# Kernel tuning notes

Hardware: AMD Instinct MI355X
Metric: run time of the kernel (lower is better)

The kernel has to match this reference:

```python
import jax, jax.numpy as jnp
import numpy as np

B, E, N, M = 512, 1024, 1024, 128
EPS = 1e-16


def setup_inputs() -> dict:
    key = jax.random.key(0)
    k1, k2, k3, k4 = jax.random.split(key, 4)
    embeddings = jax.random.normal(k1, (B, E), dtype=jnp.float32)
    w_prev = jax.random.uniform(k2, (B, N), dtype=jnp.float32)
    w_prev = w_prev / jnp.sum(w_prev, axis=1, keepdims=True)  # valid attention over N slots
    memory = jax.random.normal(k3, (B, N, M), dtype=jnp.float32)
    W = jax.random.normal(k4, (E, M + 6), dtype=jnp.float32) * (1.4 / np.sqrt(0.5 * (E + M + 6)))
    b = jnp.zeros((M + 6,), dtype=jnp.float32)
    return {"embeddings": embeddings, "w_prev": w_prev, "memory": memory, "W": W, "b": b}


def reference(embeddings, w_prev, memory, W, b):
    # Dense projection to (k | beta | g | s | y), widths (M, 1, 1, 3, 1)
    params = embeddings @ W + b  # [B, M+6]
    k = params[:, :M]                       # content key [B, M]
    beta = jax.nn.softplus(params[:, M:M + 1])   # key strength >= 0
    g = jax.nn.sigmoid(params[:, M + 1:M + 2])   # interpolation gate in (0,1)
    s = jax.nn.softmax(params[:, M + 2:M + 5], axis=1)  # shift weights [B, 3]
    y = 1.0 + jax.nn.softplus(params[:, M + 5:M + 6])   # sharpening >= 1

    # Content addressing: cosine similarity of key vs each memory row
    dot = jnp.einsum('bm,bnm->bn', k, memory)  # [B, N]
    k_norm = jnp.linalg.norm(k, axis=1, keepdims=True)          # [B, 1]
    m_norm = jnp.linalg.norm(memory, axis=2)                    # [B, N]
    cos = dot / (k_norm * m_norm + EPS)
    w_c = jax.nn.softmax(beta * cos, axis=1)  # [B, N]

    # Interpolate with previous weighting
    w_g = g * w_c + (1.0 - g) * w_prev

    # Circular convolution with 3-tap shift kernel (shifts -1, 0, +1)
    w_tilde = (s[:, 0:1] * jnp.roll(w_g, 1, axis=1)
               + s[:, 1:2] * w_g
               + s[:, 2:3] * jnp.roll(w_g, -1, axis=1))

    # Sharpen
    w_pow = jnp.power(w_tilde + EPS, y)
    w = w_pow / jnp.sum(w_pow, axis=1, keepdims=True)  # memory_locations [B, N]

    # Memory read: weighted sum of rows
    memory_data = jnp.einsum('bn,bnm->bm', w, memory)  # [B, M]
    return (memory_data, w)
```

## Files before the change

### kernel.cpp

```cpp
#include <hip/hip_runtime.h>
#include <hip/hip_bf16.h>

#define B_ 512
#define E_ 1024
#define N_ 1024
#define M_ 128
#define P_ 134

#define RLO 24
#define LLO 18

__device__ __forceinline__ float softplus_f(float x) {
    return fmaxf(x, 0.f) + log1pf(expf(-fabsf(x)));
}

__global__ __launch_bounds__(256) void k_params(
    const float* __restrict__ emb, const float* __restrict__ W,
    const float* __restrict__ bias,
    float* __restrict__ k_all, float* __restrict__ knorm,
    float* __restrict__ scal)
{
    __shared__ float se[E_];
    __shared__ float sp[P_];
    __shared__ float red[2];
    const int b = blockIdx.x, t = threadIdx.x;
    for (int i = t; i < E_; i += 256) se[i] = emb[b * E_ + i];
    __syncthreads();
    if (t < P_) {
        float a0 = 0.f, a1 = 0.f, a2 = 0.f, a3 = 0.f;
        #pragma unroll 4
        for (int e = 0; e < E_; e += 4) {
            a0 = fmaf(se[e + 0], W[(e + 0) * P_ + t], a0);
            a1 = fmaf(se[e + 1], W[(e + 1) * P_ + t], a1);
            a2 = fmaf(se[e + 2], W[(e + 2) * P_ + t], a2);
            a3 = fmaf(se[e + 3], W[(e + 3) * P_ + t], a3);
        }
        sp[t] = bias[t] + ((a0 + a1) + (a2 + a3));
    }
    __syncthreads();
    if (t < 64) {
        float v = sp[t] * sp[t] + sp[t + 64] * sp[t + 64];
        #pragma unroll
        for (int m = 1; m < 64; m <<= 1) v += __shfl_xor(v, m);
        if (t == 0) red[0] = v;
    }
    __syncthreads();
    if (t < M_) k_all[b * M_ + t] = sp[t];
    if (t == 0) {
        knorm[b] = sqrtf(red[0]);
        float beta = softplus_f(sp[M_ + 0]);
        float g    = 1.f / (1.f + expf(-sp[M_ + 1]));
        float a0 = sp[M_ + 2], a1 = sp[M_ + 3], a2 = sp[M_ + 4];
        float mx = fmaxf(a0, fmaxf(a1, a2));
        float e0 = expf(a0 - mx), e1 = expf(a1 - mx), e2 = expf(a2 - mx);
        float inv = 1.f / (e0 + e1 + e2);
        float y = 1.f + softplus_f(sp[M_ + 5]);
        float* sc = &scal[b * 8];
        sc[0] = beta; sc[1] = g; sc[2] = e0 * inv; sc[3] = e1 * inv;
        sc[4] = e2 * inv; sc[5] = y;
    }
}

__global__ __launch_bounds__(1024) void k_fused(
    const float* __restrict__ mem, const float* __restrict__ w_prev,
    const float* __restrict__ k_all, const float* __restrict__ knorm,
    const float* __restrict__ scal,
    float* __restrict__ out_md, float* __restrict__ out_w)
{
    __shared__ float zbuf[N_];
    __shared__ float wgbuf[N_];
    __shared__ float red[16];
    __shared__ float4 acc16[16][32];
    __shared__ float cache[6][32][M_];

    const int b    = blockIdx.x;
    const int t    = threadIdx.x;
    const int wid  = t >> 6;
    const int lane = t & 63;
    const int half = lane >> 5, q = lane & 31;

    const float4 k4   = *(const float4*)&k_all[b * M_ + q * 4];
    const float  kn   = knorm[b];
    const float  beta = scal[b * 8 + 0];
    const float  g    = scal[b * 8 + 1];
    const float  s0   = scal[b * 8 + 2];
    const float  s1   = scal[b * 8 + 3];
    const float  s2   = scal[b * 8 + 4];
    const float  y    = scal[b * 8 + 5];

    const float* base = mem + ((size_t)b * N_ + wid * 64 + half) * M_ + q * 4;
    float4 rc[8];

    #pragma unroll 6
    for (int i = 0; i < LLO; ++i) {
        const float4 v = *(const float4*)(base + (size_t)i * 2 * M_);
        float dot = v.x * k4.x + v.y * k4.y + v.z * k4.z + v.w * k4.w;
        float sq  = v.x * v.x + v.y * v.y + v.z * v.z + v.w * v.w;
        #pragma unroll
        for (int m = 1; m < 32; m <<= 1) {
            dot += __shfl_xor(dot, m);
            sq  += __shfl_xor(sq,  m);
        }
        if (q == 0)
            zbuf[wid * 64 + 2 * i + half] = beta * dot / (kn * sqrtf(sq) + 1e-16f);
    }
    #pragma unroll
    for (int i = LLO; i < RLO; ++i) {
        const float4 v = *(const float4*)(base + (size_t)i * 2 * M_);
        *(float4*)&cache[i - LLO][wid * 2 + half][q * 4] = v;
        float dot = v.x * k4.x + v.y * k4.y + v.z * k4.z + v.w * k4.w;
        float sq  = v.x * v.x + v.y * v.y + v.z * v.z + v.w * v.w;
        #pragma unroll
        for (int m = 1; m < 32; m <<= 1) {
            dot += __shfl_xor(dot, m);
            sq  += __shfl_xor(sq,  m);
        }
        if (q == 0)
            zbuf[wid * 64 + 2 * i + half] = beta * dot / (kn * sqrtf(sq) + 1e-16f);
    }
    #pragma unroll
    for (int ii = 0; ii < 8; ++ii) {
        const int i = RLO + ii;
        const float4 v = *(const float4*)(base + (size_t)i * 2 * M_);
        rc[ii] = v;
        float dot = v.x * k4.x + v.y * k4.y + v.z * k4.z + v.w * k4.w;
        float sq  = v.x * v.x + v.y * v.y + v.z * v.z + v.w * v.w;
        #pragma unroll
        for (int m = 1; m < 32; m <<= 1) {
            dot += __shfl_xor(dot, m);
            sq  += __shfl_xor(sq,  m);
        }
        if (q == 0)
            zbuf[wid * 64 + 2 * i + half] = beta * dot / (kn * sqrtf(sq) + 1e-16f);
    }
    __syncthreads();

    float zv = zbuf[t];
    float v = zv;
    #pragma unroll
    for (int m = 1; m < 64; m <<= 1) v = fmaxf(v, __shfl_xor(v, m));
    if (lane == 0) red[wid] = v;
    __syncthreads();
    float mx = red[0];
    #pragma unroll
    for (int j = 1; j < 16; ++j) mx = fmaxf(mx, red[j]);
    float ev = expf(zv - mx);
    v = ev;
    #pragma unroll
    for (int m = 1; m < 64; m <<= 1) v += __shfl_xor(v, m);
    __syncthreads();
    if (lane == 0) red[wid] = v;
    __syncthreads();
    float esum = 0.f;
    #pragma unroll
    for (int j = 0; j < 16; ++j) esum += red[j];
    float wc = ev / esum;
    wgbuf[t] = g * wc + (1.f - g) * w_prev[b * N_ + t];
    __syncthreads();
    float wt = s0 * wgbuf[(t - 1) & (N_ - 1)] + s1 * wgbuf[t] + s2 * wgbuf[(t + 1) & (N_ - 1)];
    float wp = powf(wt + 1e-16f, y);
    v = wp;
    #pragma unroll
    for (int m = 1; m < 64; m <<= 1) v += __shfl_xor(v, m);
    __syncthreads();
    if (lane == 0) red[wid] = v;
    __syncthreads();
    float psum = 0.f;
    #pragma unroll
    for (int j = 0; j < 16; ++j) psum += red[j];
    float wfin = wp / psum;
    zbuf[t] = wfin;
    out_w[b * N_ + t] = wfin;
    __syncthreads();

    float4 acc = make_float4(0.f, 0.f, 0.f, 0.f);
    #pragma unroll
    for (int ii = 7; ii >= 0; --ii) {
        float wv = zbuf[wid * 64 + 2 * (RLO + ii) + half];
        acc.x = fmaf(wv, rc[ii].x, acc.x);
        acc.y = fmaf(wv, rc[ii].y, acc.y);
        acc.z = fmaf(wv, rc[ii].z, acc.z);
        acc.w = fmaf(wv, rc[ii].w, acc.w);
    }
    #pragma unroll
    for (int i = RLO - 1; i >= LLO; --i) {
        float wv = zbuf[wid * 64 + 2 * i + half];
        const float4 mv = *(const float4*)&cache[i - LLO][wid * 2 + half][q * 4];
        acc.x = fmaf(wv, mv.x, acc.x);
        acc.y = fmaf(wv, mv.y, acc.y);
        acc.z = fmaf(wv, mv.z, acc.z);
        acc.w = fmaf(wv, mv.w, acc.w);
    }
    #pragma unroll 6
    for (int i = LLO - 1; i >= 0; --i) {
        float wv = zbuf[wid * 64 + 2 * i + half];
        const float4 mv = *(const float4*)(base + (size_t)i * 2 * M_);
        acc.x = fmaf(wv, mv.x, acc.x);
        acc.y = fmaf(wv, mv.y, acc.y);
        acc.z = fmaf(wv, mv.z, acc.z);
        acc.w = fmaf(wv, mv.w, acc.w);
    }
    acc.x += __shfl_xor(acc.x, 32);
    acc.y += __shfl_xor(acc.y, 32);
    acc.z += __shfl_xor(acc.z, 32);
    acc.w += __shfl_xor(acc.w, 32);
    if (lane < 32) acc16[wid][q] = acc;
    __syncthreads();
    if (t < 32) {
        float4 s = acc16[0][t];
        #pragma unroll
        for (int j = 1; j < 16; ++j) {
            float4 u = acc16[j][t];
            s.x += u.x; s.y += u.y; s.z += u.z; s.w += u.w;
        }
        *(float4*)&out_md[b * M_ + t * 4] = s;
    }
}

extern "C" void kernel_launch(void* const* d_in, const int* in_sizes, int n_in,
                              void* d_out, int out_size, void* d_ws, size_t ws_size,
                              hipStream_t stream) {
    const float* emb    = (const float*)d_in[0];
    const float* w_prev = (const float*)d_in[1];
    const float* mem    = (const float*)d_in[2];
    const float* W      = (const float*)d_in[3];
    const float* bias   = (const float*)d_in[4];

    float* out_md = (float*)d_out;
    float* out_w  = (float*)d_out + B_ * M_;

    float* ws    = (float*)d_ws;
    float* k_all = ws;
    float* knorm = ws + 65536;
    float* scal  = ws + 66048;

    k_params<<<B_, 256, 0, stream>>>(emb, W, bias, k_all, knorm, scal);
    k_fused <<<B_, 1024, 0, stream>>>(mem, w_prev, k_all, knorm, scal, out_md, out_w);
}
```

Baseline: 427.3 us.

## Fuse parameter projection into main kernel with split-K across threads

Removes the separate projection kernel and computes the dense projection inside each block of the fused kernel. The E dimension is split into four segments across 536 threads and reduced through shared memory. Derived scalars stay in shared memory instead of a global workspace. This saves a launch and the workspace round trip and parallelizes the projection more. The cost is a serialized projection phase before memory streaming in each block, plus extra shared memory.

```diff
diff --git a/kernel.cpp b/kernel.cpp
--- a/kernel.cpp
+++ b/kernel.cpp
@@ -14,59 +14,16 @@
     return fmaxf(x, 0.f) + log1pf(expf(-fabsf(x)));
 }
 
-__global__ __launch_bounds__(256) void k_params(
+__global__ __launch_bounds__(1024) void k_fused(
     const float* __restrict__ emb, const float* __restrict__ W,
-    const float* __restrict__ bias,
-    float* __restrict__ k_all, float* __restrict__ knorm,
-    float* __restrict__ scal)
+    const float* __restrict__ bias, const float* __restrict__ w_prev,
+    const float* __restrict__ mem,
+    float* __restrict__ out_md, float* __restrict__ out_w)
 {
     __shared__ float se[E_];
-    __shared__ float sp[P_];
-    __shared__ float red[2];
-    const int b = blockIdx.x, t = threadIdx.x;
-    for (int i = t; i < E_; i += 256) se[i] = emb[b * E_ + i];
-    __syncthreads();
-    if (t < P_) {
-        float a0 = 0.f, a1 = 0.f, a2 = 0.f, a3 = 0.f;
-        #pragma unroll 4
-        for (int e = 0; e < E_; e += 4) {
-            a0 = fmaf(se[e + 0], W[(e + 0) * P_ + t], a0);
-            a1 = fmaf(se[e + 1], W[(e + 1) * P_ + t], a1);
-            a2 = fmaf(se[e + 2], W[(e + 2) * P_ + t], a2);
-            a3 = fmaf(se[e + 3], W[(e + 3) * P_ + t], a3);
-        }
-        sp[t] = bias[t] + ((a0 + a1) + (a2 + a3));
-    }
-    __syncthreads();
-    if (t < 64) {
-        float v = sp[t] * sp[t] + sp[t + 64] * sp[t + 64];
-        #pragma unroll
-        for (int m = 1; m < 64; m <<= 1) v += __shfl_xor(v, m);
-        if (t == 0) red[0] = v;
-    }
-    __syncthreads();
-    if (t < M_) k_all[b * M_ + t] = sp[t];
-    if (t == 0) {
-        knorm[b] = sqrtf(red[0]);
-        float beta = softplus_f(sp[M_ + 0]);
-        float g    = 1.f / (1.f + expf(-sp[M_ + 1]));
-        float a0 = sp[M_ + 2], a1 = sp[M_ + 3], a2 = sp[M_ + 4];
-        float mx = fmaxf(a0, fmaxf(a1, a2));
-        float e0 = expf(a0 - mx), e1 = expf(a1 - mx), e2 = expf(a2 - mx);
-        float inv = 1.f / (e0 + e1 + e2);
-        float y = 1.f + softplus_f(sp[M_ + 5]);
-        float* sc = &scal[b * 8];
-        sc[0] = beta; sc[1] = g; sc[2] = e0 * inv; sc[3] = e1 * inv;
-        sc[4] = e2 * inv; sc[5] = y;
-    }
-}
-
-__global__ __launch_bounds__(1024) void k_fused(
-    const float* __restrict__ mem, const float* __restrict__ w_prev,
-    const float* __restrict__ k_all, const float* __restrict__ knorm,
-    const float* __restrict__ scal,
-    float* __restrict__ out_md, float* __restrict__ out_w)
-{
+    __shared__ float partial[4][136];
+    __shared__ float sp[136];
+    __shared__ float sscal[8];
     __shared__ float zbuf[N_];
     __shared__ float wgbuf[N_];
     __shared__ float red[16];
@@ -79,14 +36,53 @@
     const int lane = t & 63;
     const int half = lane >> 5, q = lane & 31;
 
-    const float4 k4   = *(const float4*)&k_all[b * M_ + q * 4];
-    const float  kn   = knorm[b];
-    const float  beta = scal[b * 8 + 0];
-    const float  g    = scal[b * 8 + 1];
-    const float  s0   = scal[b * 8 + 2];
-    const float  s1   = scal[b * 8 + 3];
-    const float  s2   = scal[b * 8 + 4];
-    const float  y    = scal[b * 8 + 5];
+    for (int i = t; i < E_; i += 1024) se[i] = emb[b * E_ + i];
+    __syncthreads();
+    if (t < 536) {
+        const int seg = t / 134;
+        const int col = t - seg * 134;
+        const int e0 = seg * 256;
+        const float* wcol = W + col;
+        float a0 = 0.f, a1 = 0.f, a2 = 0.f, a3 = 0.f;
+        #pragma unroll 4
+        for (int e = 0; e < 256; e += 4) {
+            a0 = fmaf(se[e0 + e + 0], wcol[(size_t)(e0 + e + 0) * P_], a0);
+            a1 = fmaf(se[e0 + e + 1], wcol[(size_t)(e0 + e + 1) * P_], a1);
+            a2 = fmaf(se[e0 + e + 2], wcol[(size_t)(e0 + e + 2) * P_], a2);
+            a3 = fmaf(se[e0 + e + 3], wcol[(size_t)(e0 + e + 3) * P_], a3);
+        }
+        partial[seg][col] = (a0 + a1) + (a2 + a3);
+    }
+    __syncthreads();
+    if (t < P_)
+        sp[t] = bias[t] + ((partial[0][t] + partial[1][t]) + (partial[2][t] + partial[3][t]));
+    __syncthreads();
+    if (t < 64) {
+        float v = sp[t] * sp[t] + sp[t + 64] * sp[t + 64];
+        #pragma unroll
+        for (int m = 1; m < 64; m <<= 1) v += __shfl_xor(v, m);
+        if (t == 0) sscal[6] = sqrtf(v);
+    }
+    if (t == 64) {
+        sscal[0] = softplus_f(sp[M_ + 0]);
+        sscal[1] = 1.f / (1.f + expf(-sp[M_ + 1]));
+        float a0 = sp[M_ + 2], a1 = sp[M_ + 3], a2 = sp[M_ + 4];
+        float mx = fmaxf(a0, fmaxf(a1, a2));
+        float e0 = expf(a0 - mx), e1 = expf(a1 - mx), e2 = expf(a2 - mx);
+        float inv = 1.f / (e0 + e1 + e2);
+        sscal[2] = e0 * inv; sscal[3] = e1 * inv; sscal[4] = e2 * inv;
+        sscal[5] = 1.f + softplus_f(sp[M_ + 5]);
+    }
+    __syncthreads();
+
+    const float4 k4   = *(const float4*)&sp[q * 4];
+    const float  kn   = sscal[6];
+    const float  beta = sscal[0];
+    const float  g    = sscal[1];
+    const float  s0   = sscal[2];
+    const float  s1   = sscal[3];
+    const float  s2   = sscal[4];
+    const float  y    = sscal[5];
 
     const float* base = mem + ((size_t)b * N_ + wid * 64 + half) * M_ + q * 4;
     float4 rc[8];
@@ -229,11 +225,5 @@
     float* out_md = (float*)d_out;
     float* out_w  = (float*)d_out + B_ * M_;
 
-    float* ws    = (float*)d_ws;
-    float* k_all = ws;
-    float* knorm = ws + 65536;
-    float* scal  = ws + 66048;
-
-    k_params<<<B_, 256, 0, stream>>>(emb, W, bias, k_all, knorm, scal);
-    k_fused <<<B_, 1024, 0, stream>>>(mem, w_prev, k_all, knorm, scal, out_md, out_w);
+    k_fused<<<B_, 1024, 0, stream>>>(emb, W, bias, w_prev, mem, out_md, out_w);
 }
```

Result: faster. 406.7 us (-4.8%).
